# Kernel optimization log

Measured on AMD Instinct MI355X. Metric: run time of the kernel, lower is better.

Reference implementation:

```python
import jax, jax.numpy as jnp
import numpy as np

CHUNK = 512
LR = 0.001  # fast-weight learning_rate


def setup_inputs() -> dict:
    key = jax.random.key(0)
    k1, k2, k3, k4 = jax.random.split(key, 4)
    B, S, H, F = 4, 4096, 1024, 4096
    x = jax.random.normal(k1, (B, S, H), dtype=jnp.float32)
    w0 = jax.random.normal(k2, (H, F), dtype=jnp.float32) * 0.02
    w1 = jax.random.normal(k3, (F, H), dtype=jnp.float32) * 0.02
    w2 = jax.random.normal(k4, (H, F), dtype=jnp.float32) * 0.02
    return {"x": x, "w0": w0, "w1": w1, "w2": w2}


def _fast_weight(xc, a0, a1, a2):
    # SwiGLU fast-weight MLP (LaCT-style): [B,C,H] -> [B,C,H]
    h = jax.nn.silu(jnp.einsum('bch,hf->bcf', xc, a0)) * jnp.einsum('bch,hf->bcf', xc, a2)
    return jnp.einsum('bcf,fh->bch', h, a1)


def reference(x, w0, w1, w2):
    B, S, H = x.shape
    nC = S // CHUNK
    # [nC, B, CHUNK, H] so scan iterates over chunks
    xc = x.reshape(B, nC, CHUNK, H).transpose(1, 0, 2, 3)

    def step(carry, x_chunk):
        a0, a1, a2, acc_loss = carry
        out = _fast_weight(x_chunk, a0, a1, a2)
        chunk_loss = jnp.mean((out - x_chunk) ** 2)
        decay = 1.0 - LR * chunk_loss  # per-chunk scalar weight decay
        return (a0 * decay, a1 * decay, a2 * decay, acc_loss + chunk_loss), out

    init = (w0, w1, w2, jnp.float32(0.0))
    (_, _, _, total_loss), outs = jax.lax.scan(step, init, xc)
    output = outs.transpose(1, 0, 2, 3).reshape(B, S, H)
    return output, total_loss / nC
```

## Files before the change

### kernel.cpp

```cpp
#include <hip/hip_runtime.h>

typedef float f32x4 __attribute__((ext_vector_type(4)));
typedef short bf16x8 __attribute__((ext_vector_type(8)));
typedef unsigned short u16;

#define B_SZ 4
#define S_SZ 4096
#define H_SZ 1024
#define F_SZ 4096
#define CHUNK_SZ 512
#define NCHUNK 8
#define MCH 2048
#define LRATE 0.001f
#define NSPLIT 4

__device__ __forceinline__ u16 f2bf(float f) {
  unsigned u = __float_as_uint(f);
  u += 0x7FFFu + ((u >> 16) & 1u);
  return (u16)(u >> 16);
}
__device__ __forceinline__ float bf2f(u16 u) {
  return __uint_as_float(((unsigned)u) << 16);
}

__device__ __forceinline__ void gload_lds16(const void* g, void* l) {
  __builtin_amdgcn_global_load_lds(
      (const __attribute__((address_space(1))) unsigned int*)g,
      (__attribute__((address_space(3))) unsigned int*)l, 16, 0, 0);
}

#define VMCNT(n) asm volatile("s_waitcnt vmcnt(" #n ")" ::: "memory")
#define SBAR() __builtin_amdgcn_s_barrier()
#define SCHED_FENCE() __builtin_amdgcn_sched_barrier(0)
#define PRIO1() __builtin_amdgcn_s_setprio(1)
#define PRIO0() __builtin_amdgcn_s_setprio(0)


__global__ __launch_bounds__(256) void k_init(float* scal) {
  if (threadIdx.x == 0) { scal[0] = 1.f; scal[1] = 0.f; }
}

__global__ __launch_bounds__(256) void k_cvt_x(const float* __restrict__ x,
                                               u16* __restrict__ xb) {
  size_t i = ((size_t)blockIdx.x * 256 + threadIdx.x) * 8;
  float4 v0 = *(const float4*)(x + i);
  float4 v1 = *(const float4*)(x + i + 4);
  union { u16 u[8]; bf16x8 v; } o;
  o.u[0] = f2bf(v0.x); o.u[1] = f2bf(v0.y); o.u[2] = f2bf(v0.z); o.u[3] = f2bf(v0.w);
  o.u[4] = f2bf(v1.x); o.u[5] = f2bf(v1.y); o.u[6] = f2bf(v1.z); o.u[7] = f2bf(v1.w);
  *(bf16x8*)(xb + i) = o.v;
}

__global__ __launch_bounds__(256) void k_transpose_cvt(const float* __restrict__ W,
                                                       u16* __restrict__ Wt,
                                                       int R, int C, int rstride, int roff) {
  __shared__ float tile[32][33];
  int tx = threadIdx.x & 31, ty = threadIdx.x >> 5;
  int r0 = blockIdx.y << 5, c0 = blockIdx.x << 5;
#pragma unroll
  for (int i = 0; i < 4; i++)
    tile[ty + i * 8][tx] = W[(size_t)(r0 + ty + i * 8) * C + c0 + tx];
  __syncthreads();
#pragma unroll
  for (int i = 0; i < 4; i++)
    Wt[((size_t)(c0 + ty + i * 8) * rstride + roff) * R + r0 + tx] = f2bf(tile[tx][ty + i * 8]);
}

__global__ __launch_bounds__(512, 2) void k_gemm_gu8(
    const u16* __restrict__ xb,
    const u16* __restrict__ wgu,
    u16* __restrict__ hbuf,
    const float* __restrict__ scal, int chunk) {
  __shared__ __align__(16) u16 sA[32768];
  __shared__ __align__(16) u16 sB[32768];

  int t = threadIdx.x;
  int lane = t & 63, wid = t >> 6;
  int wm = wid >> 2, wn = wid & 3;

  int orig = blockIdx.x;
  int wg = (orig & 7) * 32 + (orig >> 3);
  int tn = wg >> 3, tm = wg & 7;

  int gm0 = tm << 8;
  int bb = gm0 >> 9;
  int pos0 = gm0 & 511;
  const u16* Abase = xb + ((size_t)bb * S_SZ + (size_t)chunk * CHUNK_SZ + pos0) * H_SZ;

  int scol = (((t & 3) ^ ((t >> 3) & 3)) << 3);
  const u16* aS = Abase + (size_t)(t >> 2) * H_SZ + scol;
  const u16* bS = wgu + ((size_t)(tn << 8) + (t >> 2)) * H_SZ + scol;

  f32x4 acc[8][4];
#pragma unroll
  for (int i = 0; i < 8; i++)
#pragma unroll
    for (int j = 0; j < 4; j++)
#pragma unroll
      for (int k = 0; k < 4; k++) acc[i][j][k] = 0.f;

  const int rslB = (((lane >> 4)) ^ (((lane & 15) >> 1) & 3)) * 16;
  const int aRowB = ((wm << 7) + (lane & 15)) * 64 + rslB;
  const int bRowB = ((wn << 6) + (lane & 15)) * 64 + rslB;

#define STA(b_, kt_, ks_) {                                                  \
    const u16* s_ = aS + (size_t)(kt_) * 64 + (ks_) * 32;                    \
    char* d_ = (char*)sA + (b_) * 32768 + (ks_) * 16384 + t * 16;            \
    gload_lds16(s_, d_);                                                     \
    gload_lds16(s_ + (size_t)128 * H_SZ, d_ + 8192); }
#define STB(b_, kt_, ks_) {                                                  \
    const u16* s_ = bS + (size_t)(kt_) * 64 + (ks_) * 32;                    \
    char* d_ = (char*)sB + (b_) * 32768 + (ks_) * 16384 + t * 16;            \
    gload_lds16(s_, d_);                                                     \
    gload_lds16(s_ + (size_t)128 * H_SZ, d_ + 8192); }

#define LDA4(b_, ks_, FRS_) { _Pragma("unroll")                              \
    for (int i_ = 0; i_ < 4; i_++)                                           \
      av[i_] = *(const bf16x8*)((const char*)sA + (b_) * 32768 +             \
                                (ks_) * 16384 + aRowB + (FRS_ + i_) * 1024); }
#define LDB4(b_, ks_) { _Pragma("unroll")                                    \
    for (int j_ = 0; j_ < 4; j_++)                                           \
      bv[j_] = *(const bf16x8*)((const char*)sB + (b_) * 32768 +             \
                                (ks_) * 16384 + bRowB + j_ * 1024); }

#define MFMA16(FRS_) { _Pragma("unroll")                                     \
    for (int i_ = 0; i_ < 4; i_++)                                           \
      _Pragma("unroll")                                                      \
      for (int j_ = 0; j_ < 4; j_++)                                         \
        acc[FRS_ + i_][j_] = __builtin_amdgcn_mfma_f32_16x16x32_bf16(        \
            av[i_], bv[j_], acc[FRS_ + i_][j_], 0, 0, 0); }

#define TILE(b_, ktn_, ST_) {                                                \
    bf16x8 av[4], bv[4];                                                     \
                            \
    LDA4(b_, 0, 0); LDB4(b_, 0);                                             \
    if (ST_) STA(b_ ^ 1, ktn_, 0);                                           \
    SBAR(); SCHED_FENCE();                                                   \
    PRIO1(); MFMA16(0); PRIO0();                                             \
    SBAR();                                                                  \
                                  \
    LDA4(b_, 0, 4);                                                          \
    if (ST_) STB(b_ ^ 1, ktn_, 0);                                           \
    SBAR(); SCHED_FENCE();                                                   \
    PRIO1(); MFMA16(4); PRIO0();                                             \
    if (ST_) { VMCNT(4); } else { VMCNT(0); }                                \
    SBAR();                                                                  \
                                                  \
    LDA4(b_, 1, 0); LDB4(b_, 1);                                             \
    if (ST_) STA(b_ ^ 1, ktn_, 1);                                           \
    SBAR(); SCHED_FENCE();                                                   \
    PRIO1(); MFMA16(0); PRIO0();                                             \
    SBAR();                                                                  \
                                                  \
    LDA4(b_, 1, 4);                                                          \
    if (ST_) STB(b_ ^ 1, ktn_, 1);                                           \
    SBAR(); SCHED_FENCE();                                                   \
    PRIO1(); MFMA16(4); PRIO0();                                             \
    if (ST_) { VMCNT(4); SBAR(); }                                           \
  }

  STA(0, 0, 0); STB(0, 0, 0); STA(0, 0, 1); STB(0, 0, 1);
  VMCNT(4);
  SBAR();

#pragma unroll 1
  for (int kt = 0; kt < 14; kt += 2) {
    TILE(0, kt + 1, 1);
    TILE(1, kt + 2, 1);
  }
  TILE(0, 15, 1);
  TILE(1, 0, 0);

  float D = scal[0];
#pragma unroll
  for (int fr = 0; fr < 8; fr++)
#pragma unroll
    for (int fc = 0; fc < 4; fc++) {
      int row0 = (tm << 8) + (wm << 7) + (fr << 4) + ((lane >> 4) << 2);
      int col = (tn << 8) + (wn << 6) + (fc << 4) + (lane & 15);
      int f = col >> 1;
#pragma unroll
      for (int j = 0; j < 4; j++) {
        float v = acc[fr][fc][j];
        float w = __shfl_xor(v, 1);
        float g = D * ((lane & 1) ? w : v);
        float u = D * ((lane & 1) ? v : w);
        float h = (g / (1.f + __expf(-g))) * u;
        if (!(lane & 1)) hbuf[(size_t)(row0 + j) * F_SZ + f] = f2bf(h);
      }
    }
}

__global__ __launch_bounds__(256, 2) void k_gemm_out(
    const u16* __restrict__ hbuf,
    const u16* __restrict__ w1t,
    u16* __restrict__ pbuf) {
  __shared__ __align__(16) u16 sA[128 * 64];
  __shared__ __align__(16) u16 sB[128 * 64];

  int t = threadIdx.x;
  int lane = t & 63, wid = t >> 6;
  int wm = wid >> 1, wn = wid & 1;

  int orig = blockIdx.x + gridDim.x * (blockIdx.y + gridDim.y * blockIdx.z);
  int nwg = gridDim.x * gridDim.y * gridDim.z;
  int wg = (orig & 7) * (nwg >> 3) + (orig >> 3);
  int tm = wg & 15;
  int tn = (wg >> 4) & 7;
  int kz = wg >> 7;

  int srow = t >> 3;
  int scol = (((t & 7) ^ (srow & 7)) << 3);
  const u16* aSrc = hbuf + ((size_t)(tm << 7) + srow) * F_SZ + kz * 1024 + scol;
  const u16* bSrc = w1t + ((size_t)(tn << 7) + srow) * F_SZ + kz * 1024 + scol;
  char* aDst = (char*)sA + t * 16;
  char* bDst = (char*)sB + t * 16;

  f32x4 acc[4][4];
#pragma unroll
  for (int i = 0; i < 4; i++)
#pragma unroll
    for (int j = 0; j < 4; j++)
#pragma unroll
      for (int k = 0; k < 4; k++) acc[i][j][k] = 0.f;

  int arow = (wm << 6) + (lane & 15);
  int brow = (wn << 6) + (lane & 15);
  int sl0 = (lane >> 4) ^ (lane & 7);
  int sl1 = ((lane >> 4) | 4) ^ (lane & 7);
  const int aO0 = arow * 128 + sl0 * 16, aO1 = arow * 128 + sl1 * 16;
  const int bO0 = brow * 128 + sl0 * 16, bO1 = brow * 128 + sl1 * 16;

#pragma unroll 1
  for (int k0 = 0; k0 < 1024; k0 += 64) {
#pragma unroll
    for (int r = 0; r < 4; r++) {
      gload_lds16(aSrc + (size_t)r * 32 * F_SZ, aDst + r * 4096);
      gload_lds16(bSrc + (size_t)r * 32 * F_SZ, bDst + r * 4096);
    }
    aSrc += 64; bSrc += 64;
    __syncthreads();

    {
      bf16x8 av[4], bv[4];
#pragma unroll
      for (int fr = 0; fr < 4; fr++) av[fr] = *(const bf16x8*)((const char*)sA + aO0 + fr * 2048);
#pragma unroll
      for (int fc = 0; fc < 4; fc++) bv[fc] = *(const bf16x8*)((const char*)sB + bO0 + fc * 2048);
#pragma unroll
      for (int fr = 0; fr < 4; fr++)
#pragma unroll
        for (int fc = 0; fc < 4; fc++)
          acc[fr][fc] = __builtin_amdgcn_mfma_f32_16x16x32_bf16(av[fr], bv[fc], acc[fr][fc], 0, 0, 0);
    }
    {
      bf16x8 av[4], bv[4];
#pragma unroll
      for (int fr = 0; fr < 4; fr++) av[fr] = *(const bf16x8*)((const char*)sA + aO1 + fr * 2048);
#pragma unroll
      for (int fc = 0; fc < 4; fc++) bv[fc] = *(const bf16x8*)((const char*)sB + bO1 + fc * 2048);
#pragma unroll
      for (int fr = 0; fr < 4; fr++)
#pragma unroll
        for (int fc = 0; fc < 4; fc++)
          acc[fr][fc] = __builtin_amdgcn_mfma_f32_16x16x32_bf16(av[fr], bv[fc], acc[fr][fc], 0, 0, 0);
    }
    __syncthreads();
  }

#pragma unroll
  for (int fr = 0; fr < 4; fr++)
#pragma unroll
    for (int fc = 0; fc < 4; fc++) {
      int row0 = (tm << 7) + (wm << 6) + (fr << 4) + ((lane >> 4) << 2);
      int col = (tn << 7) + (wn << 6) + (fc << 4) + (lane & 15);
#pragma unroll
      for (int j = 0; j < 4; j++)
        pbuf[((size_t)kz * MCH + row0 + j) * 1024 + col] = f2bf(acc[fr][fc][j]);
    }
}

__global__ __launch_bounds__(256) void k_epilogue(
    const u16* __restrict__ pbuf, const float* __restrict__ x,
    float* __restrict__ out, const float* __restrict__ scal,
    float* __restrict__ partials, int chunk) {
  __shared__ float red[256];
  int t = threadIdx.x;
  size_t base = ((size_t)blockIdx.x * 256 + t) * 8;
  int row = (int)(base >> 10);
  int col = (int)(base & 1023);
  float D = scal[0];

  float s[8] = {0.f, 0.f, 0.f, 0.f, 0.f, 0.f, 0.f, 0.f};
#pragma unroll
  for (int kz = 0; kz < NSPLIT; kz++) {
    union { bf16x8 v; u16 u[8]; } p;
    p.v = *(const bf16x8*)(pbuf + (size_t)kz * MCH * 1024 + base);
#pragma unroll
    for (int j = 0; j < 8; j++) s[j] += bf2f(p.u[j]);
  }

  int bb = row >> 9, pos = row & 511;
  size_t off = ((size_t)bb * S_SZ + (size_t)chunk * CHUNK_SZ + pos) * H_SZ + col;
  float4 x0 = *(const float4*)(x + off);
  float4 x1 = *(const float4*)(x + off + 4);
  float xv[8] = {x0.x, x0.y, x0.z, x0.w, x1.x, x1.y, x1.z, x1.w};
  float ov[8];
  float psum = 0.f;
#pragma unroll
  for (int j = 0; j < 8; j++) {
    ov[j] = D * s[j];
    float e = ov[j] - xv[j];
    psum += e * e;
  }
  *(float4*)(out + off) = make_float4(ov[0], ov[1], ov[2], ov[3]);
  *(float4*)(out + off + 4) = make_float4(ov[4], ov[5], ov[6], ov[7]);

  red[t] = psum;
  __syncthreads();
  for (int s2 = 128; s2 > 0; s2 >>= 1) {
    if (t < s2) red[t] += red[t + s2];
    __syncthreads();
  }
  if (t == 0) partials[blockIdx.x] = red[0];
}

__global__ __launch_bounds__(256) void k_update(float* scal, const float* __restrict__ partials,
                                                float* lossout, int chunk) {
  __shared__ float red[256];
  int t = threadIdx.x;
  float s = 0.f;
  for (int i = t; i < 1024; i += 256) s += partials[i];
  red[t] = s;
  __syncthreads();
  for (int s2 = 128; s2 > 0; s2 >>= 1) {
    if (t < s2) red[t] += red[t + s2];
    __syncthreads();
  }
  if (t == 0) {
    float loss = red[0] / (float)((size_t)MCH * H_SZ);
    float total = scal[1] + loss;
    scal[1] = total;
    scal[0] = scal[0] * (1.f - LRATE * loss);
    if (chunk == NCHUNK - 1) lossout[0] = total / (float)NCHUNK;
  }
}

extern "C" void kernel_launch(void* const* d_in, const int* in_sizes, int n_in,
                              void* d_out, int out_size, void* d_ws, size_t ws_size,
                              hipStream_t stream) {
  const float* x = (const float*)d_in[0];
  const float* w0 = (const float*)d_in[1];
  const float* w1 = (const float*)d_in[2];
  const float* w2 = (const float*)d_in[3];
  float* out = (float*)d_out;

  char* ws = (char*)d_ws;
  float* scal = (float*)ws;
  float* partials = (float*)(ws + 1024);
  u16* xb = (u16*)(ws + 8192);
  u16* wgu = xb + (size_t)B_SZ * S_SZ * H_SZ;
  u16* w1t = wgu + (size_t)8192 * 1024;
  u16* hbuf = w1t + (size_t)F_SZ * H_SZ;
  u16* pbuf = hbuf + (size_t)MCH * F_SZ;

  k_init<<<1, 256, 0, stream>>>(scal);
  k_cvt_x<<<(B_SZ * S_SZ * H_SZ) / (256 * 8), 256, 0, stream>>>(x, xb);
  k_transpose_cvt<<<dim3(F_SZ / 32, H_SZ / 32), 256, 0, stream>>>(w0, wgu, H_SZ, F_SZ, 2, 0);
  k_transpose_cvt<<<dim3(F_SZ / 32, H_SZ / 32), 256, 0, stream>>>(w2, wgu, H_SZ, F_SZ, 2, 1);
  k_transpose_cvt<<<dim3(H_SZ / 32, F_SZ / 32), 256, 0, stream>>>(w1, w1t, F_SZ, H_SZ, 1, 0);

  float* lossout = out + (size_t)B_SZ * S_SZ * H_SZ;
  for (int c = 0; c < NCHUNK; c++) {
    k_gemm_gu8<<<dim3(256), 512, 0, stream>>>(xb, wgu, hbuf, scal, c);
    k_gemm_out<<<dim3(16, 8, NSPLIT), 256, 0, stream>>>(hbuf, w1t, pbuf);
    k_epilogue<<<1024, 256, 0, stream>>>(pbuf, x, out, scal, partials, c);
    k_update<<<1, 256, 0, stream>>>(scal, partials, lossout, c);
  }
}
```

Baseline: 652.2 us.

## Restructure gate/up GEMM tile pipeline and fold per-chunk decay into consumers

Rewrites the gate/up GEMM main loop to use a wider 128-byte K slab per LDS row with an 8-way swizzle, a different warp-to-fragment mapping, and a new four-phase prefetch and barrier schedule. It also changes launch bounds to one block per CU. The scalar state kernels (init and per-chunk update) are removed: each consumer recomputes the decay product from per-chunk partial sums, and a single final kernel reduces the loss. This drops two launches per chunk but adds redundant partial-sum reductions in every block, and the lower occupancy hint may reduce latency hiding.

New measurement: 613.9 us. 5.9% less time.

```diff
diff --git a/kernel.cpp b/kernel.cpp
--- a/kernel.cpp
+++ b/kernel.cpp
@@ -13,6 +13,7 @@
 #define MCH 2048
 #define LRATE 0.001f
 #define NSPLIT 4
+#define NELEM_F 2097152.0f
 
 __device__ __forceinline__ u16 f2bf(float f) {
   unsigned u = __float_as_uint(f);
@@ -34,11 +35,8 @@
 #define SCHED_FENCE() __builtin_amdgcn_sched_barrier(0)
 #define PRIO1() __builtin_amdgcn_s_setprio(1)
 #define PRIO0() __builtin_amdgcn_s_setprio(0)
-
-
-__global__ __launch_bounds__(256) void k_init(float* scal) {
-  if (threadIdx.x == 0) { scal[0] = 1.f; scal[1] = 0.f; }
-}
+#define MFMA(a, b, c) __builtin_amdgcn_mfma_f32_16x16x32_bf16((a), (b), (c), 0, 0, 0)
+
 
 __global__ __launch_bounds__(256) void k_cvt_x(const float* __restrict__ x,
                                                u16* __restrict__ xb) {
@@ -66,13 +64,15 @@
     Wt[((size_t)(c0 + ty + i * 8) * rstride + roff) * R + r0 + tx] = f2bf(tile[tx][ty + i * 8]);
 }
 
-__global__ __launch_bounds__(512, 2) void k_gemm_gu8(
+__global__ __launch_bounds__(512, 1) void k_gemm_gu8(
     const u16* __restrict__ xb,
     const u16* __restrict__ wgu,
     u16* __restrict__ hbuf,
-    const float* __restrict__ scal, int chunk) {
+    const float* __restrict__ partials,
+    int chunk) {
   __shared__ __align__(16) u16 sA[32768];
   __shared__ __align__(16) u16 sB[32768];
+  __shared__ float lossL[8];
 
   int t = threadIdx.x;
   int lane = t & 63, wid = t >> 6;
@@ -87,9 +87,9 @@
   int pos0 = gm0 & 511;
   const u16* Abase = xb + ((size_t)bb * S_SZ + (size_t)chunk * CHUNK_SZ + pos0) * H_SZ;
 
-  int scol = (((t & 3) ^ ((t >> 3) & 3)) << 3);
-  const u16* aS = Abase + (size_t)(t >> 2) * H_SZ + scol;
-  const u16* bS = wgu + ((size_t)(tn << 8) + (t >> 2)) * H_SZ + scol;
+  int swz = (((t & 7) ^ ((t >> 3) & 7)) << 3);
+  const u16* aS = Abase + (size_t)(t >> 3) * H_SZ + swz;
+  const u16* bS = wgu + ((size_t)(tn << 8) + (t >> 3)) * H_SZ + swz;
 
   f32x4 acc[8][4];
 #pragma unroll
@@ -99,85 +99,114 @@
 #pragma unroll
       for (int k = 0; k < 4; k++) acc[i][j][k] = 0.f;
 
-  const int rslB = (((lane >> 4)) ^ (((lane & 15) >> 1) & 3)) * 16;
-  const int aRowB = ((wm << 7) + (lane & 15)) * 64 + rslB;
-  const int bRowB = ((wn << 6) + (lane & 15)) * 64 + rslB;
-
-#define STA(b_, kt_, ks_) {                                                  \
-    const u16* s_ = aS + (size_t)(kt_) * 64 + (ks_) * 32;                    \
-    char* d_ = (char*)sA + (b_) * 32768 + (ks_) * 16384 + t * 16;            \
+  const int aRow = ((wm << 6) + (lane & 15)) * 128;
+  const int bRow = ((wn << 5) + (lane & 15)) * 128;
+  const int s0 = (((lane >> 4)) ^ (lane & 7)) * 16;
+  const int s1 = (((lane >> 4) | 4) ^ (lane & 7)) * 16;
+
+#define STA(b_, kn_, h_) {                                                   \
+    const u16* s_ = aS + (size_t)(h_) * 128 * H_SZ + (size_t)(kn_) * 64;     \
+    char* d_ = (char*)sA + (b_) * 32768 + (h_) * 16384 + t * 16;             \
     gload_lds16(s_, d_);                                                     \
-    gload_lds16(s_ + (size_t)128 * H_SZ, d_ + 8192); }
-#define STB(b_, kt_, ks_) {                                                  \
-    const u16* s_ = bS + (size_t)(kt_) * 64 + (ks_) * 32;                    \
-    char* d_ = (char*)sB + (b_) * 32768 + (ks_) * 16384 + t * 16;            \
+    gload_lds16(s_ + (size_t)64 * H_SZ, d_ + 8192); }
+#define STB(b_, kn_, h_) {                                                   \
+    const u16* s_ = bS + (size_t)(h_) * 128 * H_SZ + (size_t)(kn_) * 64;     \
+    char* d_ = (char*)sB + (b_) * 32768 + (h_) * 16384 + t * 16;             \
     gload_lds16(s_, d_);                                                     \
-    gload_lds16(s_ + (size_t)128 * H_SZ, d_ + 8192); }
-
-#define LDA4(b_, ks_, FRS_) { _Pragma("unroll")                              \
-    for (int i_ = 0; i_ < 4; i_++)                                           \
-      av[i_] = *(const bf16x8*)((const char*)sA + (b_) * 32768 +             \
-                                (ks_) * 16384 + aRowB + (FRS_ + i_) * 1024); }
-#define LDB4(b_, ks_) { _Pragma("unroll")                                    \
-    for (int j_ = 0; j_ < 4; j_++)                                           \
-      bv[j_] = *(const bf16x8*)((const char*)sB + (b_) * 32768 +             \
-                                (ks_) * 16384 + bRowB + j_ * 1024); }
-
-#define MFMA16(FRS_) { _Pragma("unroll")                                     \
-    for (int i_ = 0; i_ < 4; i_++)                                           \
-      _Pragma("unroll")                                                      \
-      for (int j_ = 0; j_ < 4; j_++)                                         \
-        acc[FRS_ + i_][j_] = __builtin_amdgcn_mfma_f32_16x16x32_bf16(        \
-            av[i_], bv[j_], acc[FRS_ + i_][j_], 0, 0, 0); }
-
-#define TILE(b_, ktn_, ST_) {                                                \
-    bf16x8 av[4], bv[4];                                                     \
-                            \
-    LDA4(b_, 0, 0); LDB4(b_, 0);                                             \
-    if (ST_) STA(b_ ^ 1, ktn_, 0);                                           \
-    SBAR(); SCHED_FENCE();                                                   \
-    PRIO1(); MFMA16(0); PRIO0();                                             \
-    SBAR();                                                                  \
-                                  \
-    LDA4(b_, 0, 4);                                                          \
-    if (ST_) STB(b_ ^ 1, ktn_, 0);                                           \
-    SBAR(); SCHED_FENCE();                                                   \
-    PRIO1(); MFMA16(4); PRIO0();                                             \
-    if (ST_) { VMCNT(4); } else { VMCNT(0); }                                \
-    SBAR();                                                                  \
-                                                  \
-    LDA4(b_, 1, 0); LDB4(b_, 1);                                             \
-    if (ST_) STA(b_ ^ 1, ktn_, 1);                                           \
-    SBAR(); SCHED_FENCE();                                                   \
-    PRIO1(); MFMA16(0); PRIO0();                                             \
-    SBAR();                                                                  \
-                                                  \
-    LDA4(b_, 1, 4);                                                          \
-    if (ST_) STB(b_ ^ 1, ktn_, 1);                                           \
-    SBAR(); SCHED_FENCE();                                                   \
-    PRIO1(); MFMA16(4); PRIO0();                                             \
-    if (ST_) { VMCNT(4); SBAR(); }                                           \
-  }
-
-  STA(0, 0, 0); STB(0, 0, 0); STA(0, 0, 1); STB(0, 0, 1);
-  VMCNT(4);
+    gload_lds16(s_ + (size_t)64 * H_SZ, d_ + 8192); }
+
+#define TILE(b_, kn_)                                                        \
+  {                                                                          \
+    const char* Ab = (const char*)sA + (b_) * 32768;                         \
+    const char* Bb = (const char*)sB + (b_) * 32768;                         \
+    bf16x8 av0[4], av1[4], b0k0[2], b0k1[2], b1k0[2], b1k1[2];               \
+     \
+    _Pragma("unroll") for (int i = 0; i < 4; i++) {                          \
+      av0[i] = *(const bf16x8*)(Ab + aRow + i * 2048 + s0);                  \
+      av1[i] = *(const bf16x8*)(Ab + aRow + i * 2048 + s1);                  \
+    }                                                                        \
+    _Pragma("unroll") for (int j = 0; j < 2; j++) {                          \
+      b0k0[j] = *(const bf16x8*)(Bb + bRow + j * 2048 + s0);                 \
+      b0k1[j] = *(const bf16x8*)(Bb + bRow + j * 2048 + s1);                 \
+    }                                                                        \
+    STA(b_ ^ 1, kn_, 0);                                                     \
+    SCHED_FENCE(); VMCNT(4); SBAR(); SCHED_FENCE();                          \
+    PRIO1();                                                                 \
+    _Pragma("unroll") for (int i = 0; i < 4; i++)                            \
+      _Pragma("unroll") for (int j = 0; j < 2; j++) {                        \
+        acc[i][j] = MFMA(av0[i], b0k0[j], acc[i][j]);                        \
+        acc[i][j] = MFMA(av1[i], b0k1[j], acc[i][j]);                        \
+      }                                                                      \
+    PRIO0();                                                                 \
+      \
+    _Pragma("unroll") for (int j = 0; j < 2; j++) {                          \
+      b1k0[j] = *(const bf16x8*)(Bb + 16384 + bRow + j * 2048 + s0);         \
+      b1k1[j] = *(const bf16x8*)(Bb + 16384 + bRow + j * 2048 + s1);         \
+    }                                                                        \
+    STB(b_ ^ 1, kn_, 0);                                                     \
+    SCHED_FENCE(); VMCNT(4); SBAR(); SCHED_FENCE();                          \
+    PRIO1();                                                                 \
+    _Pragma("unroll") for (int i = 0; i < 4; i++)                            \
+      _Pragma("unroll") for (int j = 0; j < 2; j++) {                        \
+        acc[i][2 + j] = MFMA(av0[i], b1k0[j], acc[i][2 + j]);                \
+        acc[i][2 + j] = MFMA(av1[i], b1k1[j], acc[i][2 + j]);                \
+      }                                                                      \
+    PRIO0();                                                                 \
+     \
+    _Pragma("unroll") for (int i = 0; i < 4; i++) {                          \
+      av0[i] = *(const bf16x8*)(Ab + 16384 + aRow + i * 2048 + s0);          \
+      av1[i] = *(const bf16x8*)(Ab + 16384 + aRow + i * 2048 + s1);          \
+    }                                                                        \
+    STB(b_ ^ 1, kn_, 1);                                                     \
+    SCHED_FENCE(); SBAR(); SCHED_FENCE();                                    \
+    PRIO1();                                                                 \
+    _Pragma("unroll") for (int i = 0; i < 4; i++)                            \
+      _Pragma("unroll") for (int j = 0; j < 2; j++) {                        \
+        acc[4 + i][j] = MFMA(av0[i], b0k0[j], acc[4 + i][j]);                \
+        acc[4 + i][j] = MFMA(av1[i], b0k1[j], acc[4 + i][j]);                \
+      }                                                                      \
+    PRIO0();                                                                 \
+                  \
+    STA(b_ ^ 1, kn_, 1);                                                     \
+    SCHED_FENCE(); VMCNT(4); SBAR(); SCHED_FENCE();                          \
+    PRIO1();                                                                 \
+    _Pragma("unroll") for (int i = 0; i < 4; i++)                            \
+      _Pragma("unroll") for (int j = 0; j < 2; j++) {                        \
+        acc[4 + i][2 + j] = MFMA(av0[i], b1k0[j], acc[4 + i][2 + j]);        \
+        acc[4 + i][2 + j] = MFMA(av1[i], b1k1[j], acc[4 + i][2 + j]);        \
+      }                                                                      \
+    PRIO0();                                                                 \
+  }
+
+  STA(0, 0, 0); STB(0, 0, 0); STB(0, 0, 1); STA(0, 0, 1);
+  VMCNT(0);
   SBAR();
 
 #pragma unroll 1
-  for (int kt = 0; kt < 14; kt += 2) {
-    TILE(0, kt + 1, 1);
-    TILE(1, kt + 2, 1);
-  }
-  TILE(0, 15, 1);
-  TILE(1, 0, 0);
-
-  float D = scal[0];
+  for (int kt = 0; kt < 16; kt += 2) {
+    TILE(0, kt + 1);
+    TILE(1, kt + 2);
+  }
+
+  __syncthreads();
+  if (wid < chunk) {
+    float s = 0.f;
+#pragma unroll
+    for (int i = 0; i < 16; i++) s += partials[wid * 1024 + lane + i * 64];
+#pragma unroll
+    for (int o = 32; o > 0; o >>= 1) s += __shfl_down(s, o);
+    if (lane == 0) lossL[wid] = s;
+  }
+  __syncthreads();
+  float D = 1.f;
+  for (int j = 0; j < chunk; j++) D *= (1.f - LRATE * (lossL[j] / NELEM_F));
+
 #pragma unroll
   for (int fr = 0; fr < 8; fr++)
 #pragma unroll
     for (int fc = 0; fc < 4; fc++) {
-      int row0 = (tm << 8) + (wm << 7) + (fr << 4) + ((lane >> 4) << 2);
-      int col = (tn << 8) + (wn << 6) + (fc << 4) + (lane & 15);
+      int row0 = (tm << 8) + ((fr >> 2) << 7) + (wm << 6) + ((fr & 3) << 4) + ((lane >> 4) << 2);
+      int col = (tn << 8) + ((fc >> 1) << 7) + (wn << 5) + ((fc & 1) << 4) + (lane & 15);
       int f = col >> 1;
 #pragma unroll
       for (int j = 0; j < 4; j++) {
@@ -282,14 +311,29 @@
 
 __global__ __launch_bounds__(256) void k_epilogue(
     const u16* __restrict__ pbuf, const float* __restrict__ x,
-    float* __restrict__ out, const float* __restrict__ scal,
-    float* __restrict__ partials, int chunk) {
+    float* __restrict__ out,
+    float* __restrict__ partials,
+    int chunk) {
   __shared__ float red[256];
+  __shared__ float lossL[8];
   int t = threadIdx.x;
+  int lane = t & 63, wid = t >> 6;
+
+  for (int j = wid; j < chunk; j += 4) {
+    float s = 0.f;
+#pragma unroll
+    for (int i = 0; i < 16; i++) s += partials[j * 1024 + lane + i * 64];
+#pragma unroll
+    for (int o = 32; o > 0; o >>= 1) s += __shfl_down(s, o);
+    if (lane == 0) lossL[j] = s;
+  }
+  __syncthreads();
+  float D = 1.f;
+  for (int j = 0; j < chunk; j++) D *= (1.f - LRATE * (lossL[j] / NELEM_F));
+
   size_t base = ((size_t)blockIdx.x * 256 + t) * 8;
   int row = (int)(base >> 10);
   int col = (int)(base & 1023);
-  float D = scal[0];
 
   float s[8] = {0.f, 0.f, 0.f, 0.f, 0.f, 0.f, 0.f, 0.f};
 #pragma unroll
@@ -322,28 +366,22 @@
     if (t < s2) red[t] += red[t + s2];
     __syncthreads();
   }
-  if (t == 0) partials[blockIdx.x] = red[0];
-}
-
-__global__ __launch_bounds__(256) void k_update(float* scal, const float* __restrict__ partials,
-                                                float* lossout, int chunk) {
+  if (t == 0) partials[chunk * 1024 + blockIdx.x] = red[0];
+}
+
+__global__ __launch_bounds__(256) void k_update_final(const float* __restrict__ partials,
+                                                      float* __restrict__ lossout) {
   __shared__ float red[256];
   int t = threadIdx.x;
   float s = 0.f;
-  for (int i = t; i < 1024; i += 256) s += partials[i];
+  for (int i = t; i < NCHUNK * 1024; i += 256) s += partials[i];
   red[t] = s;
   __syncthreads();
   for (int s2 = 128; s2 > 0; s2 >>= 1) {
     if (t < s2) red[t] += red[t + s2];
     __syncthreads();
   }
-  if (t == 0) {
-    float loss = red[0] / (float)((size_t)MCH * H_SZ);
-    float total = scal[1] + loss;
-    scal[1] = total;
-    scal[0] = scal[0] * (1.f - LRATE * loss);
-    if (chunk == NCHUNK - 1) lossout[0] = total / (float)NCHUNK;
-  }
+  if (t == 0) lossout[0] = (red[0] / NELEM_F) / (float)NCHUNK;
 }
 
 extern "C" void kernel_launch(void* const* d_in, const int* in_sizes, int n_in,
@@ -356,15 +394,13 @@
   float* out = (float*)d_out;
 
   char* ws = (char*)d_ws;
-  float* scal = (float*)ws;
-  float* partials = (float*)(ws + 1024);
-  u16* xb = (u16*)(ws + 8192);
+  float* partials = (float*)ws;
+  u16* xb = (u16*)(ws + 40960);
   u16* wgu = xb + (size_t)B_SZ * S_SZ * H_SZ;
   u16* w1t = wgu + (size_t)8192 * 1024;
   u16* hbuf = w1t + (size_t)F_SZ * H_SZ;
   u16* pbuf = hbuf + (size_t)MCH * F_SZ;
 
-  k_init<<<1, 256, 0, stream>>>(scal);
   k_cvt_x<<<(B_SZ * S_SZ * H_SZ) / (256 * 8), 256, 0, stream>>>(x, xb);
   k_transpose_cvt<<<dim3(F_SZ / 32, H_SZ / 32), 256, 0, stream>>>(w0, wgu, H_SZ, F_SZ, 2, 0);
   k_transpose_cvt<<<dim3(F_SZ / 32, H_SZ / 32), 256, 0, stream>>>(w2, wgu, H_SZ, F_SZ, 2, 1);
@@ -372,9 +408,9 @@
 
   float* lossout = out + (size_t)B_SZ * S_SZ * H_SZ;
   for (int c = 0; c < NCHUNK; c++) {
-    k_gemm_gu8<<<dim3(256), 512, 0, stream>>>(xb, wgu, hbuf, scal, c);
+    k_gemm_gu8<<<dim3(256), 512, 0, stream>>>(xb, wgu, hbuf, partials, c);
     k_gemm_out<<<dim3(16, 8, NSPLIT), 256, 0, stream>>>(hbuf, w1t, pbuf);
-    k_epilogue<<<1024, 256, 0, stream>>>(pbuf, x, out, scal, partials, c);
-    k_update<<<1, 256, 0, stream>>>(scal, partials, lossout, c);
-  }
-}
+    k_epilogue<<<1024, 256, 0, stream>>>(pbuf, x, out, partials, c);
+  }
+  k_update_final<<<1, 256, 0, stream>>>(partials, lossout);
+}
```
